# Optimization experiments

Measured on AMD Instinct MI355X. Metric: run time of the kernel, lower is better.

## Reference

```python
import jax, jax.numpy as jnp
import numpy as np

N, M, NBR = 20000, 12, 64
AF, ORIG, H, B, K = 256, 92, 256, 200, 50
N_CONV = 3
EPS = 1e-5


def _bn_train(x, gamma, beta):
    mu = x.mean(0)
    var = x.var(0)  # biased, matches torch BN normalization in train mode
    return (x - mu) * jax.lax.rsqrt(var + EPS) * gamma + beta


def _conv_layer(atom_in, nbr_fea, nbr_idx, w1, b1, w2, b2, gamma, beta):
    n, m = nbr_idx.shape
    m1 = m // 2
    atom_nbr = atom_in[nbr_idx]                     # [N, M, AF]
    atom_u = jnp.broadcast_to(atom_in[:, None, :], (n, m1, atom_in.shape[-1]))
    an1, an2 = atom_nbr[:, :m1], atom_nbr[:, m1:]
    nf1, nf2 = nbr_fea[:, :m1], nbr_fea[:, m1:]
    u1 = jnp.concatenate([atom_u, an1, nf1], axis=2)  # [N, M1, 2*AF+NBR]
    u2 = jnp.concatenate([atom_u, an2, nf2], axis=2)
    g1 = jax.nn.relu(jnp.einsum('nmf,fo->nmo', u1, w1) + b1)
    g2 = jax.nn.softplus(jnp.einsum('nmf,fo->nmo', u2, w1) + b1)
    nbr_sumed = g1.sum(1) + g2.sum(1)               # sum over all M neighbors, [N, 2*AF]
    nbr_sumed = nbr_sumed @ w2 + b2                 # [N, AF]
    nbr_sumed = _bn_train(nbr_sumed, gamma, beta)
    return jax.nn.softplus(atom_in + nbr_sumed)


def setup_inputs() -> dict:
    key = jax.random.key(0)
    ks = jax.random.split(key, 16)
    inp = {
        'atom_fea': jax.random.normal(ks[0], (N, ORIG), jnp.float32),
        'nbr_fea': jax.random.normal(ks[1], (N, M, NBR), jnp.float32),
        'nbr_fea_idx': jax.random.randint(ks[2], (N, M), 0, N),
        'M1_index': jax.random.randint(ks[3], (B * K,), 0, N),
        'seg_ids': jnp.repeat(jnp.arange(B), K),
        'm2_fea': jax.random.normal(ks[4], (B, 4), jnp.float32),
        'emb_w': jax.random.normal(ks[5], (ORIG, AF), jnp.float32) * 0.05,
        'emb_b': jnp.zeros((AF,), jnp.float32),
        'w1': jax.random.normal(ks[6], (N_CONV, 2 * AF + NBR, 2 * AF), jnp.float32) * 0.05,
        'b1': jnp.zeros((N_CONV, 2 * AF), jnp.float32),
        'w2': jax.random.normal(ks[7], (N_CONV, 2 * AF, AF), jnp.float32) * 0.05,
        'b2': jnp.zeros((N_CONV, AF), jnp.float32),
        'gamma': jnp.ones((N_CONV, AF), jnp.float32),
        'beta': jnp.zeros((N_CONV, AF), jnp.float32),
        'fc_w': jax.random.normal(ks[8], (AF + 4, H), jnp.float32) * 0.05,
        'fc_b': jnp.zeros((H,), jnp.float32),
        'out_w': jax.random.normal(ks[9], (H, 1), jnp.float32) * 0.05,
        'out_b': jnp.zeros((1,), jnp.float32),
    }
    return inp


def reference(atom_fea, nbr_fea, nbr_fea_idx, M1_index, seg_ids, m2_fea,
              emb_w, emb_b, w1, b1, w2, b2, gamma, beta,
              fc_w, fc_b, out_w, out_b):
    x = jax.nn.softplus(atom_fea @ emb_w + emb_b)           # [N, AF]
    for i in range(N_CONV):
        x = _conv_layer(x, nbr_fea, nbr_fea_idx, w1[i], b1[i], w2[i], b2[i], gamma[i], beta[i])
    m1_fea = x[M1_index]                                    # [B*K, AF]
    sums = jax.ops.segment_sum(m1_fea, seg_ids, num_segments=B)
    counts = jax.ops.segment_sum(jnp.ones((m1_fea.shape[0], 1), m1_fea.dtype), seg_ids, num_segments=B)
    crys = sums / counts                                    # per-crystal mean, [B, AF]
    crys = jnp.concatenate([crys, m2_fea], axis=1)          # [B, AF+4]
    h = jax.nn.softplus(jax.nn.softplus(crys) @ fc_w + fc_b)
    out = h @ out_w + out_b                                 # [B, 1]
    return out
```

## Files before the change

kernel.cpp:

```cpp
#include <hip/hip_runtime.h>
#include <hip/hip_bf16.h>


#define N_ATOM 20000
#define AF     256
#define F2     512
#define ORIG   92
#define ORIG_P 96
#define BB     200
#define KK     50
#define BN_EPS 1e-5f
#define ZS     132

#define OFF_B1   0
#define OFF_B2   1536
#define OFF_GAM  2304
#define OFF_BET  3072
#define OFF_EMBB 3840
#define OFF_FCB  4096
#define OFF_FCW  4352
#define OFF_OW   70912
#define OFF_OB   71168
#define OFF_M2   71169
#define N_SMALL  71969

using bf16x8 = __attribute__((ext_vector_type(8))) short;
using f32x4  = __attribute__((ext_vector_type(4))) float;

__device__ __forceinline__ float bf2f(__hip_bfloat16 v) { return __bfloat162float(v); }
__device__ __forceinline__ __hip_bfloat16 f2bf(float v) { return __float2bfloat16(v); }
__device__ __forceinline__ unsigned short f2bfbits(float f) {
    unsigned u = __float_as_uint(f);
    u += 0x7fffu + ((u >> 16) & 1u);
    return (unsigned short)(u >> 16);
}
__device__ __forceinline__ float bfbits2f(unsigned short u) {
    return __uint_as_float(((unsigned)u) << 16);
}
__device__ __forceinline__ float softplus_f(float x) {
    return fmaxf(x, 0.f) + __logf(1.f + __expf(-fabsf(x)));
}
__device__ __forceinline__ float ld_any(const void* p, long idx, bool isf32) {
    return isf32 ? ((const float*)p)[idx] : bf2f(((const __hip_bfloat16*)p)[idx]);
}

__global__ void detect_dtype(const unsigned* __restrict__ gamma_raw,
                             unsigned* __restrict__ flag) {
    unsigned u = gamma_raw[0];
    flag[0] = ((u & 0xFFFFu) == 0u) ? 1u : 0u;
}

__global__ __launch_bounds__(256) void prep_nf(const void* __restrict__ nf,
                                               const unsigned* __restrict__ dflag,
                                               unsigned* __restrict__ out) {
    bool isf32 = dflag[0] != 0u;
    int idx = blockIdx.x * 256 + threadIdx.x;
    if (idx >= N_ATOM * 12 * 64 / 4) return;
    if (isf32) {
        float4 v = ((const float4*)nf)[idx];
        out[idx * 2]     = (unsigned)f2bfbits(v.x) | ((unsigned)f2bfbits(v.y) << 16);
        out[idx * 2 + 1] = (unsigned)f2bfbits(v.z) | ((unsigned)f2bfbits(v.w) << 16);
    } else {
        uint2 v = ((const uint2*)nf)[idx];
        ((uint2*)out)[idx] = v;
    }
}

__global__ __launch_bounds__(256) void prep_pad_af(const void* __restrict__ af,
                                                   const unsigned* __restrict__ dflag,
                                                   __hip_bfloat16* __restrict__ out) {
    bool isf32 = dflag[0] != 0u;
    int i = blockIdx.x * 256 + threadIdx.x;
    if (i >= N_ATOM * ORIG_P) return;
    int r = i / ORIG_P, k = i - r * ORIG_P;
    out[i] = (k < ORIG) ? f2bf(ld_any(af, (long)r * ORIG + k, isf32)) : f2bf(0.f);
}
__global__ __launch_bounds__(256) void prep_t_emb(const void* __restrict__ w,
                                                  const unsigned* __restrict__ dflag,
                                                  __hip_bfloat16* __restrict__ out) {
    bool isf32 = dflag[0] != 0u;
    int i = blockIdx.x * 256 + threadIdx.x;
    if (i >= AF * ORIG_P) return;
    int n = i / ORIG_P, k = i - n * ORIG_P;
    out[i] = (k < ORIG) ? f2bf(ld_any(w, (long)k * AF + n, isf32)) : f2bf(0.f);
}
__global__ __launch_bounds__(256) void prep_t_w1(const void* __restrict__ w,
                                                 const unsigned* __restrict__ dflag,
                                                 __hip_bfloat16* __restrict__ out) {
    bool isf32 = dflag[0] != 0u;
    int i = blockIdx.x * 256 + threadIdx.x;
    if (i >= 3 * F2 * 576) return;
    int l = i / (F2 * 576); int rem = i - l * (F2 * 576);
    int c = rem / 576, k = rem - c * 576;
    out[i] = f2bf(ld_any(w, (long)l * 576 * F2 + (long)k * F2 + c, isf32));
}
__global__ __launch_bounds__(256) void prep_t_w2(const void* __restrict__ w,
                                                 const unsigned* __restrict__ dflag,
                                                 __hip_bfloat16* __restrict__ out) {
    bool isf32 = dflag[0] != 0u;
    int i = blockIdx.x * 256 + threadIdx.x;
    if (i >= 3 * AF * F2) return;
    int l = i / (AF * F2); int rem = i - l * (AF * F2);
    int n = rem / F2, k = rem - n * F2;
    out[i] = f2bf(ld_any(w, (long)l * F2 * AF + (long)k * AF + n, isf32));
}
__global__ __launch_bounds__(256)
void prep_smalls(const void* b1, const void* b2, const void* gam, const void* bet,
                 const void* embb, const void* fcb, const void* fcw,
                 const void* ow, const void* ob, const void* m2,
                 const unsigned* __restrict__ dflag,
                 __hip_bfloat16* __restrict__ s) {
    bool isf32 = dflag[0] != 0u;
    int i = blockIdx.x * 256 + threadIdx.x;
    if (i >= N_SMALL) return;
    float v;
    if      (i < OFF_B2)   v = ld_any(b1,   i - OFF_B1,  isf32);
    else if (i < OFF_GAM)  v = ld_any(b2,   i - OFF_B2,  isf32);
    else if (i < OFF_BET)  v = ld_any(gam,  i - OFF_GAM, isf32);
    else if (i < OFF_EMBB) v = ld_any(bet,  i - OFF_BET, isf32);
    else if (i < OFF_FCB)  v = ld_any(embb, i - OFF_EMBB,isf32);
    else if (i < OFF_OW)   v = (i < OFF_FCW) ? ld_any(fcb, i - OFF_FCB, isf32)
                                             : ld_any(fcw, i - OFF_FCW, isf32);
    else if (i < OFF_OB)   v = ld_any(ow,   i - OFF_OW,  isf32);
    else if (i < OFF_M2)   v = ld_any(ob,   i - OFF_OB,  isf32);
    else                   v = ld_any(m2,   i - OFF_M2,  isf32);
    s[i] = f2bf(v);
}

template <bool OUT_BF16>
__global__ __launch_bounds__(256)
void gemm_kernel(const __hip_bfloat16* __restrict__ A, int lda,
                 const __hip_bfloat16* __restrict__ BT, int ldb,
                 void* __restrict__ Cp, int M, int N, int K,
                 const __hip_bfloat16* __restrict__ bias, int act,
                 float* __restrict__ st) {
    __shared__ __align__(16) unsigned short sA[128 * 40];
    __shared__ __align__(16) unsigned short sB[128 * 40];
    __shared__ float sS[128], sS2[128];
    int tid  = threadIdx.x;
    int mt   = blockIdx.x, nt = blockIdx.y;
    int wave = tid >> 6, lane = tid & 63, q = lane >> 4, ln = lane & 15;
    int wr   = wave >> 1, wc = wave & 1;

    if (st && tid < 128) { sS[tid] = 0.f; sS2[tid] = 0.f; }

    f32x4 acc[4][4];
    for (int i = 0; i < 4; i++)
        for (int j = 0; j < 4; j++) acc[i][j] = (f32x4){0.f, 0.f, 0.f, 0.f};

    for (int k0 = 0; k0 < K; k0 += 32) {
        for (int i = tid; i < 512; i += 256) {
            int r = i >> 2, ch = i & 3;
            int row = mt * 128 + r;
            uint4 va = make_uint4(0u, 0u, 0u, 0u);
            if (row < M) va = *(const uint4*)(A + (size_t)row * lda + k0 + ch * 8);
            *(uint4*)(&sA[r * 40 + ch * 8]) = va;
            int n = nt * 128 + r;
            uint4 vb = *(const uint4*)(BT + (size_t)n * ldb + k0 + ch * 8);
            *(uint4*)(&sB[r * 40 + ch * 8]) = vb;
        }
        __syncthreads();
        bf16x8 af[4], bf[4];
        for (int i = 0; i < 4; i++)
            af[i] = *(const bf16x8*)(&sA[(wr * 64 + i * 16 + ln) * 40 + q * 8]);
        for (int j = 0; j < 4; j++)
            bf[j] = *(const bf16x8*)(&sB[(wc * 64 + j * 16 + ln) * 40 + q * 8]);
        for (int i = 0; i < 4; i++)
            for (int j = 0; j < 4; j++)
                acc[i][j] = __builtin_amdgcn_mfma_f32_16x16x32_bf16(af[i], bf[j], acc[i][j], 0, 0, 0);
        __syncthreads();
    }
    for (int j = 0; j < 4; j++) {
        int cl  = wc * 64 + j * 16 + ln;
        int col = nt * 128 + cl;
        float bv = bias ? bf2f(bias[col]) : 0.f;
        float ls = 0.f, ls2 = 0.f;
        for (int i = 0; i < 4; i++) {
            for (int r = 0; r < 4; r++) {
                int row = mt * 128 + wr * 64 + i * 16 + q * 4 + r;
                if (row >= M) continue;
                float v = acc[i][j][r] + bv;
                if (st) { ls += v; ls2 += v * v; }
                if (act == 1) v = softplus_f(v);
                if (OUT_BF16) ((__hip_bfloat16*)Cp)[(size_t)row * N + col] = f2bf(v);
                else          ((float*)Cp)[(size_t)row * N + col] = v;
            }
        }
        if (st) { atomicAdd(&sS[cl], ls); atomicAdd(&sS2[cl], ls2); }
    }
    if (st) {
        __syncthreads();
        if (tid < 128) {
            int col = nt * 128 + tid;
            atomicAdd(&st[col], sS[tid]);
            atomicAdd(&st[AF + col], sS2[tid]);
        }
    }
}

__global__ __launch_bounds__(256)
void conv_fused(const void* __restrict__ nf,
                const unsigned* __restrict__ dflag,
                int prepped,
                const int* __restrict__ nidx,
                const __hip_bfloat16* __restrict__ xa,
                const __hip_bfloat16* __restrict__ y,
                const __hip_bfloat16* __restrict__ w1Tl,
                __hip_bfloat16* __restrict__ ns)
{
    __shared__ __align__(16) unsigned short sNF[96 * 72];
    __shared__ __align__(16) unsigned short sR[96 * ZS];
    __shared__ int sIdx[96];
    unsigned short* sBT = sR;
    unsigned short* sZ  = sR;

    int tid = threadIdx.x;
    int ab  = blockIdx.x * 8;

    if (prepped || dflag[0] == 0u) {
        const __hip_bfloat16* nfB = (const __hip_bfloat16*)nf;
        for (int i = tid; i < 96 * 8; i += 256) {
            int r = i >> 3, ch = i & 7;
            uint4 v = *(const uint4*)(nfB + (size_t)(ab * 12 + r) * 64 + ch * 8);
            *(uint4*)(&sNF[r * 72 + ch * 8]) = v;
        }
    } else {
        const float* nfF = (const float*)nf;
        for (int i = tid; i < 96 * 8; i += 256) {
            int r = i >> 3, ch = i & 7;
            const float* src = nfF + (size_t)(ab * 12 + r) * 64 + ch * 8;
            float4 v0 = *(const float4*)(src);
            float4 v1 = *(const float4*)(src + 4);
            unsigned short* d = &sNF[r * 72 + ch * 8];
            d[0] = f2bfbits(v0.x); d[1] = f2bfbits(v0.y);
            d[2] = f2bfbits(v0.z); d[3] = f2bfbits(v0.w);
            d[4] = f2bfbits(v1.x); d[5] = f2bfbits(v1.y);
            d[6] = f2bfbits(v1.z); d[7] = f2bfbits(v1.w);
        }
    }
    if (tid < 96) sIdx[tid] = nidx[ab * 12 + tid];

    int wave = tid >> 6, lane = tid & 63, q = lane >> 4, ln = lane & 15;
    int c0 = wave * 32;
    int a  = tid >> 5, chc = tid & 31;
    int n  = ab + a;

    for (int ct = 0; ct < 4; ct++) {
        int cb = ct * 128;
        __syncthreads();
        for (int i = tid; i < 128 * 8; i += 256) {
            int c = i >> 3, ch = i & 7;
            uint4 v = *(const uint4*)(w1Tl + (size_t)(cb + c) * 576 + 512 + ch * 8);
            *(uint4*)(&sBT[c * 72 + ch * 8]) = v;
        }
        __syncthreads();

        bf16x8 bfr[2][2];
        for (int c2 = 0; c2 < 2; c2++)
            for (int ks = 0; ks < 2; ks++)
                bfr[c2][ks] = *(const bf16x8*)(&sBT[(c0 + c2 * 16 + ln) * 72 + ks * 32 + q * 8]);

        f32x4 acc[6][2];
        for (int rt = 0; rt < 6; rt++)
            for (int c2 = 0; c2 < 2; c2++) acc[rt][c2] = (f32x4){0.f, 0.f, 0.f, 0.f};
        for (int rt = 0; rt < 6; rt++) {
            bf16x8 a0 = *(const bf16x8*)(&sNF[(rt * 16 + ln) * 72 + q * 8]);
            bf16x8 a1 = *(const bf16x8*)(&sNF[(rt * 16 + ln) * 72 + 32 + q * 8]);
            acc[rt][0] = __builtin_amdgcn_mfma_f32_16x16x32_bf16(a0, bfr[0][0], acc[rt][0], 0, 0, 0);
            acc[rt][0] = __builtin_amdgcn_mfma_f32_16x16x32_bf16(a1, bfr[0][1], acc[rt][0], 0, 0, 0);
            acc[rt][1] = __builtin_amdgcn_mfma_f32_16x16x32_bf16(a0, bfr[1][0], acc[rt][1], 0, 0, 0);
            acc[rt][1] = __builtin_amdgcn_mfma_f32_16x16x32_bf16(a1, bfr[1][1], acc[rt][1], 0, 0, 0);
        }
        __syncthreads();

        for (int rt = 0; rt < 6; rt++)
            for (int c2 = 0; c2 < 2; c2++)
                for (int r = 0; r < 4; r++)
                    sZ[(rt * 16 + q * 4 + r) * ZS + c0 + c2 * 16 + ln] = f2bfbits(acc[rt][c2][r]);
        __syncthreads();

        int gc = cb + chc * 4;
        uint2 xau = *(const uint2*)(xa + (size_t)n * F2 + gc);
        float xa0 = bfbits2f((unsigned short)(xau.x & 0xffff));
        float xa1 = bfbits2f((unsigned short)(xau.x >> 16));
        float xa2 = bfbits2f((unsigned short)(xau.y & 0xffff));
        float xa3 = bfbits2f((unsigned short)(xau.y >> 16));
        float r0 = 0.f, r1 = 0.f, r2 = 0.f, r3 = 0.f;
#pragma unroll
        for (int m = 0; m < 12; m++) {
            int gi = sIdx[a * 12 + m];
            uint2 zz = *(const uint2*)(&sZ[(a * 12 + m) * ZS + chc * 4]);
            uint2 yy = *(const uint2*)(y + (size_t)gi * F2 + gc);
            float v0 = bfbits2f((unsigned short)(zz.x & 0xffff)) + xa0 +
                       bfbits2f((unsigned short)(yy.x & 0xffff));
            float v1 = bfbits2f((unsigned short)(zz.x >> 16)) + xa1 +
                       bfbits2f((unsigned short)(yy.x >> 16));
            float v2 = bfbits2f((unsigned short)(zz.y & 0xffff)) + xa2 +
                       bfbits2f((unsigned short)(yy.y & 0xffff));
            float v3 = bfbits2f((unsigned short)(zz.y >> 16)) + xa3 +
                       bfbits2f((unsigned short)(yy.y >> 16));
            if (m < 6) {
                v0 = fmaxf(v0, 0.f); v1 = fmaxf(v1, 0.f);
                v2 = fmaxf(v2, 0.f); v3 = fmaxf(v3, 0.f);
            } else {
                v0 = softplus_f(v0); v1 = softplus_f(v1);
                v2 = softplus_f(v2); v3 = softplus_f(v3);
            }
            r0 += v0; r1 += v1; r2 += v2; r3 += v3;
        }
        uint2 o;
        o.x = (unsigned)f2bfbits(r0) | ((unsigned)f2bfbits(r1) << 16);
        o.y = (unsigned)f2bfbits(r2) | ((unsigned)f2bfbits(r3) << 16);
        *(uint2*)(ns + (size_t)n * F2 + gc) = o;
    }
}

__global__ __launch_bounds__(256)
void bn_apply(const __hip_bfloat16* __restrict__ h2, const float* __restrict__ st,
              const __hip_bfloat16* __restrict__ x,
              const __hip_bfloat16* __restrict__ gamma,
              const __hip_bfloat16* __restrict__ beta,
              __hip_bfloat16* __restrict__ xo) {
    int i = (blockIdx.x * 256 + threadIdx.x) * 4;
    int c = i & 255;
    uint2 hv = *(const uint2*)(h2 + i);
    uint2 xv = *(const uint2*)(x + i);
    uint2 o;
    float r[4];
#pragma unroll
    for (int k = 0; k < 4; k++) {
        int cc = c + k;
        float mu  = st[cc] * (1.f / 20000.f);
        float var = fmaxf(st[AF + cc] * (1.f / 20000.f) - mu * mu, 0.f);
        unsigned hh = (k < 2) ? hv.x : hv.y;
        unsigned xx = (k < 2) ? xv.x : xv.y;
        float h = bfbits2f((unsigned short)((k & 1) ? (hh >> 16) : (hh & 0xffff)));
        float xf = bfbits2f((unsigned short)((k & 1) ? (xx >> 16) : (xx & 0xffff)));
        float t = (h - mu) * rsqrtf(var + BN_EPS) * bf2f(gamma[cc]) + bf2f(beta[cc]);
        r[k] = softplus_f(xf + t);
    }
    o.x = (unsigned)f2bfbits(r[0]) | ((unsigned)f2bfbits(r[1]) << 16);
    o.y = (unsigned)f2bfbits(r[2]) | ((unsigned)f2bfbits(r[3]) << 16);
    *(uint2*)(xo + i) = o;
}

__global__ __launch_bounds__(256)
void readout(const __hip_bfloat16* __restrict__ x, const int* __restrict__ m1,
             const __hip_bfloat16* __restrict__ smalls,
             const unsigned* __restrict__ dflag,
             void* __restrict__ outp) {
    __shared__ float sc[AF + 4];
    __shared__ float sred[4];
    bool isf32 = dflag[0] != 0u;
    int b = blockIdx.x, tid = threadIdx.x;
    float s = 0.f;
    for (int j = 0; j < KK; j++) {
        int row = m1[b * KK + j];
        s += bf2f(x[(size_t)row * AF + tid]);
    }
    sc[tid] = softplus_f(s * (1.f / (float)KK));
    if (tid < 4) sc[AF + tid] = softplus_f(bf2f(smalls[OFF_M2 + b * 4 + tid]));
    __syncthreads();
    float acc = bf2f(smalls[OFF_FCB + tid]);
    for (int k = 0; k < AF + 4; k++) acc += sc[k] * bf2f(smalls[OFF_FCW + k * 256 + tid]);
    float h = softplus_f(acc);
    float v = h * bf2f(smalls[OFF_OW + tid]);
    for (int off = 32; off > 0; off >>= 1) v += __shfl_down(v, off);
    if ((tid & 63) == 0) sred[tid >> 6] = v;
    __syncthreads();
    if (tid == 0) {
        float o = sred[0] + sred[1] + sred[2] + sred[3] + bf2f(smalls[OFF_OB]);
        if (isf32) ((float*)outp)[b] = o;
        else       ((__hip_bfloat16*)outp)[b] = f2bf(o);
    }
}

extern "C" void kernel_launch(void* const* d_in, const int* in_sizes, int n_in,
                              void* d_out, int out_size, void* d_ws, size_t ws_size,
                              hipStream_t stream) {
    const void* atom_fea = d_in[0];
    const void* nbr_fea  = d_in[1];
    const int*  nbr_idx  = (const int*)d_in[2];
    const int*  m1_idx   = (const int*)d_in[3];
    const void* m2_fea = d_in[5];
    const void* emb_w  = d_in[6];
    const void* emb_b  = d_in[7];
    const void* w1     = d_in[8];
    const void* b1     = d_in[9];
    const void* w2     = d_in[10];
    const void* b2     = d_in[11];
    const void* gamma  = d_in[12];
    const void* beta   = d_in[13];
    const void* fc_w   = d_in[14];
    const void* fc_b   = d_in[15];
    const void* out_w  = d_in[16];
    const void* out_b  = d_in[17];

    char* ws = (char*)d_ws;
    size_t off = 0;
    auto alloc = [&](size_t bytes) -> char* {
        char* p = ws + off;
        off += (bytes + 255) & ~(size_t)255;
        return p;
    };
    __hip_bfloat16* w1T    = (__hip_bfloat16*)alloc((size_t)3 * F2 * 576 * 2);
    __hip_bfloat16* w2T    = (__hip_bfloat16*)alloc((size_t)3 * AF * F2 * 2);
    __hip_bfloat16* smalls = (__hip_bfloat16*)alloc((size_t)N_SMALL * 2);
    __hip_bfloat16* xb0    = (__hip_bfloat16*)alloc((size_t)N_ATOM * AF * 2);
    __hip_bfloat16* xb1    = (__hip_bfloat16*)alloc((size_t)N_ATOM * AF * 2);
    char*           regX   = alloc((size_t)N_ATOM * F2 * 2);
    char*           regY   = alloc((size_t)N_ATOM * F2 * 2);
    char*           regZ   = alloc((size_t)N_ATOM * F2 * 2);
    float*          stats  = (float*)alloc((size_t)3 * 2 * AF * 4);
    unsigned*       dflag  = (unsigned*)alloc(256);
    char*           nfb    = alloc((size_t)N_ATOM * 12 * 64 * 2);
    int use_nfb = (ws_size >= off) ? 1 : 0;

    __hip_bfloat16* xa     = (__hip_bfloat16*)regX;
    __hip_bfloat16* h2     = (__hip_bfloat16*)regX;
    __hip_bfloat16* af_pad = (__hip_bfloat16*)regY;
    __hip_bfloat16* yb     = (__hip_bfloat16*)regY;
    __hip_bfloat16* embT   = (__hip_bfloat16*)regZ;
    __hip_bfloat16* nsb    = (__hip_bfloat16*)regZ;

    detect_dtype<<<1, 1, 0, stream>>>((const unsigned*)gamma, dflag);
    (void)hipMemsetAsync(stats, 0, (size_t)3 * 2 * AF * 4, stream);

    if (use_nfb)
        prep_nf<<<(N_ATOM * 12 * 64 / 4 + 255) / 256, 256, 0, stream>>>(nbr_fea, dflag,
                                                                        (unsigned*)nfb);
    prep_pad_af<<<(N_ATOM * ORIG_P + 255) / 256, 256, 0, stream>>>(atom_fea, dflag, af_pad);
    prep_t_emb<<<(AF * ORIG_P + 255) / 256, 256, 0, stream>>>(emb_w, dflag, embT);
    prep_t_w1<<<(3 * F2 * 576 + 255) / 256, 256, 0, stream>>>(w1, dflag, w1T);
    prep_t_w2<<<(3 * AF * F2 + 255) / 256, 256, 0, stream>>>(w2, dflag, w2T);
    prep_smalls<<<(N_SMALL + 255) / 256, 256, 0, stream>>>(b1, b2, gamma, beta, emb_b,
                                                           fc_b, fc_w, out_w, out_b, m2_fea,
                                                           dflag, smalls);

    dim3 g_emb((N_ATOM + 127) / 128, AF / 128);
    gemm_kernel<true><<<g_emb, 256, 0, stream>>>(af_pad, ORIG_P, embT, ORIG_P,
                                                 xb0, N_ATOM, AF, ORIG_P,
                                                 smalls + OFF_EMBB, 1, nullptr);

    const void* nf_conv = use_nfb ? (const void*)nfb : nbr_fea;

    __hip_bfloat16* xc = xb0;
    __hip_bfloat16* xn = xb1;
    for (int l = 0; l < 3; l++) {
        const __hip_bfloat16* w1Tl = w1T + (size_t)l * F2 * 576;
        dim3 gxy((N_ATOM + 127) / 128, F2 / 128);
        gemm_kernel<true><<<gxy, 256, 0, stream>>>(xc, AF, w1Tl, 576,
                                                   xa, N_ATOM, F2, AF,
                                                   smalls + OFF_B1 + l * F2, 0, nullptr);
        gemm_kernel<true><<<gxy, 256, 0, stream>>>(xc, AF, w1Tl + 256, 576,
                                                   yb, N_ATOM, F2, AF, nullptr, 0, nullptr);
        conv_fused<<<N_ATOM / 8, 256, 0, stream>>>(nf_conv, dflag, use_nfb, nbr_idx,
                                                   xa, yb, w1Tl, nsb);
        float* stl = stats + l * 2 * AF;
        dim3 gh2((N_ATOM + 127) / 128, AF / 128);
        gemm_kernel<true><<<gh2, 256, 0, stream>>>(nsb, F2, w2T + (size_t)l * AF * F2, F2,
                                                   h2, N_ATOM, AF, F2,
                                                   smalls + OFF_B2 + l * AF, 0, stl);
        bn_apply<<<(N_ATOM * AF / 4) / 256, 256, 0, stream>>>(h2, stl, xc,
                                                              smalls + OFF_GAM + l * AF,
                                                              smalls + OFF_BET + l * AF, xn);
        __hip_bfloat16* t = xc; xc = xn; xn = t;
    }
    readout<<<BB, 256, 0, stream>>>(xc, m1_idx, smalls, dflag, d_out);
}
```

Baseline: 646.4 us.

## Merge prep kernels, fuse dual node GEMMs into one, shrink conv block

Replaces the separate weight and feature prep kernels with a single prep_all launch. The two per-layer node GEMMs (self and neighbor projections) become one GEMM with N=1024 that writes an interleaved xa|y buffer. The bias add moves into conv_fused. The conv kernel now handles 4 atoms per block instead of 8 and reads the nbr_fea projection weights directly from a pre-packed global layout instead of staging them in shared memory. The separate nbr_fea bf16 conversion pass is dropped, so fp32 inputs are converted inside conv on every layer, and the smaller blocks lower shared-memory use in exchange for more blocks.

```diff
diff --git a/kernel.cpp b/kernel.cpp
--- a/kernel.cpp
+++ b/kernel.cpp
@@ -24,6 +24,14 @@
 #define OFF_M2   71169
 #define N_SMALL  71969
 
+#define S_AF   (N_ATOM * ORIG_P)
+#define S_EMB  (AF * ORIG_P)
+#define S_W12  (3 * 1024 * 256)
+#define S_W1F  (3 * 512 * 64)
+#define S_W2   (3 * AF * F2)
+#define S_SM   N_SMALL
+#define S_TOT  (S_AF + S_EMB + S_W12 + S_W1F + S_W2 + S_SM)
+
 using bf16x8 = __attribute__((ext_vector_type(8))) short;
 using f32x4  = __attribute__((ext_vector_type(4))) float;
 
@@ -50,69 +58,53 @@
     flag[0] = ((u & 0xFFFFu) == 0u) ? 1u : 0u;
 }
 
-__global__ __launch_bounds__(256) void prep_nf(const void* __restrict__ nf,
-                                               const unsigned* __restrict__ dflag,
-                                               unsigned* __restrict__ out) {
-    bool isf32 = dflag[0] != 0u;
-    int idx = blockIdx.x * 256 + threadIdx.x;
-    if (idx >= N_ATOM * 12 * 64 / 4) return;
-    if (isf32) {
-        float4 v = ((const float4*)nf)[idx];
-        out[idx * 2]     = (unsigned)f2bfbits(v.x) | ((unsigned)f2bfbits(v.y) << 16);
-        out[idx * 2 + 1] = (unsigned)f2bfbits(v.z) | ((unsigned)f2bfbits(v.w) << 16);
-    } else {
-        uint2 v = ((const uint2*)nf)[idx];
-        ((uint2*)out)[idx] = v;
-    }
-}
-
-__global__ __launch_bounds__(256) void prep_pad_af(const void* __restrict__ af,
-                                                   const unsigned* __restrict__ dflag,
-                                                   __hip_bfloat16* __restrict__ out) {
+__global__ __launch_bounds__(256)
+void prep_all(const void* af, const void* emb_w, const void* w1, const void* w2,
+              const void* b1, const void* b2, const void* gam, const void* bet,
+              const void* embb, const void* fcb, const void* fcw,
+              const void* ow, const void* ob, const void* m2,
+              const unsigned* __restrict__ dflag,
+              __hip_bfloat16* __restrict__ af_pad, __hip_bfloat16* __restrict__ embT,
+              __hip_bfloat16* __restrict__ w1T2, __hip_bfloat16* __restrict__ w1Tf,
+              __hip_bfloat16* __restrict__ w2T, __hip_bfloat16* __restrict__ smalls) {
     bool isf32 = dflag[0] != 0u;
     int i = blockIdx.x * 256 + threadIdx.x;
-    if (i >= N_ATOM * ORIG_P) return;
-    int r = i / ORIG_P, k = i - r * ORIG_P;
-    out[i] = (k < ORIG) ? f2bf(ld_any(af, (long)r * ORIG + k, isf32)) : f2bf(0.f);
-}
-__global__ __launch_bounds__(256) void prep_t_emb(const void* __restrict__ w,
-                                                  const unsigned* __restrict__ dflag,
-                                                  __hip_bfloat16* __restrict__ out) {
-    bool isf32 = dflag[0] != 0u;
-    int i = blockIdx.x * 256 + threadIdx.x;
-    if (i >= AF * ORIG_P) return;
-    int n = i / ORIG_P, k = i - n * ORIG_P;
-    out[i] = (k < ORIG) ? f2bf(ld_any(w, (long)k * AF + n, isf32)) : f2bf(0.f);
-}
-__global__ __launch_bounds__(256) void prep_t_w1(const void* __restrict__ w,
-                                                 const unsigned* __restrict__ dflag,
-                                                 __hip_bfloat16* __restrict__ out) {
-    bool isf32 = dflag[0] != 0u;
-    int i = blockIdx.x * 256 + threadIdx.x;
-    if (i >= 3 * F2 * 576) return;
-    int l = i / (F2 * 576); int rem = i - l * (F2 * 576);
-    int c = rem / 576, k = rem - c * 576;
-    out[i] = f2bf(ld_any(w, (long)l * 576 * F2 + (long)k * F2 + c, isf32));
-}
-__global__ __launch_bounds__(256) void prep_t_w2(const void* __restrict__ w,
-                                                 const unsigned* __restrict__ dflag,
-                                                 __hip_bfloat16* __restrict__ out) {
-    bool isf32 = dflag[0] != 0u;
-    int i = blockIdx.x * 256 + threadIdx.x;
-    if (i >= 3 * AF * F2) return;
-    int l = i / (AF * F2); int rem = i - l * (AF * F2);
-    int n = rem / F2, k = rem - n * F2;
-    out[i] = f2bf(ld_any(w, (long)l * F2 * AF + (long)k * AF + n, isf32));
-}
-__global__ __launch_bounds__(256)
-void prep_smalls(const void* b1, const void* b2, const void* gam, const void* bet,
-                 const void* embb, const void* fcb, const void* fcw,
-                 const void* ow, const void* ob, const void* m2,
-                 const unsigned* __restrict__ dflag,
-                 __hip_bfloat16* __restrict__ s) {
-    bool isf32 = dflag[0] != 0u;
-    int i = blockIdx.x * 256 + threadIdx.x;
-    if (i >= N_SMALL) return;
+    if (i < S_AF) {
+        int r = i / ORIG_P, k = i - r * ORIG_P;
+        af_pad[i] = (k < ORIG) ? f2bf(ld_any(af, (long)r * ORIG + k, isf32)) : f2bf(0.f);
+        return;
+    }
+    i -= S_AF;
+    if (i < S_EMB) {
+        int n = i / ORIG_P, k = i - n * ORIG_P;
+        embT[i] = (k < ORIG) ? f2bf(ld_any(emb_w, (long)k * AF + n, isf32)) : f2bf(0.f);
+        return;
+    }
+    i -= S_EMB;
+    if (i < S_W12) {
+        int l = i / (1024 * 256); int rem = i - l * (1024 * 256);
+        int c = rem / 256, k = rem - c * 256;
+        long src = (c < 512) ? ((long)(l * 576 + k) * F2 + c)
+                             : ((long)(l * 576 + 256 + k) * F2 + (c - 512));
+        w1T2[i] = f2bf(ld_any(w1, src, isf32));
+        return;
+    }
+    i -= S_W12;
+    if (i < S_W1F) {
+        int l = i / (512 * 64); int rem = i - l * (512 * 64);
+        int c = rem / 64, k = rem - c * 64;
+        w1Tf[i] = f2bf(ld_any(w1, (long)(l * 576 + 512 + k) * F2 + c, isf32));
+        return;
+    }
+    i -= S_W1F;
+    if (i < S_W2) {
+        int l = i / (AF * F2); int rem = i - l * (AF * F2);
+        int n = rem / F2, k = rem - n * F2;
+        w2T[i] = f2bf(ld_any(w2, (long)(l * F2 + k) * AF + n, isf32));
+        return;
+    }
+    i -= S_W2;
+    if (i >= S_SM) return;
     float v;
     if      (i < OFF_B2)   v = ld_any(b1,   i - OFF_B1,  isf32);
     else if (i < OFF_GAM)  v = ld_any(b2,   i - OFF_B2,  isf32);
@@ -124,14 +116,14 @@
     else if (i < OFF_OB)   v = ld_any(ow,   i - OFF_OW,  isf32);
     else if (i < OFF_M2)   v = ld_any(ob,   i - OFF_OB,  isf32);
     else                   v = ld_any(m2,   i - OFF_M2,  isf32);
-    s[i] = f2bf(v);
+    smalls[i] = f2bf(v);
 }
 
 template <bool OUT_BF16>
 __global__ __launch_bounds__(256)
 void gemm_kernel(const __hip_bfloat16* __restrict__ A, int lda,
                  const __hip_bfloat16* __restrict__ BT, int ldb,
-                 void* __restrict__ Cp, int M, int N, int K,
+                 void* __restrict__ Cp, int M, int ldc, int K,
                  const __hip_bfloat16* __restrict__ bias, int act,
                  float* __restrict__ st) {
     __shared__ __align__(16) unsigned short sA[128 * 40];
@@ -182,8 +174,8 @@
                 float v = acc[i][j][r] + bv;
                 if (st) { ls += v; ls2 += v * v; }
                 if (act == 1) v = softplus_f(v);
-                if (OUT_BF16) ((__hip_bfloat16*)Cp)[(size_t)row * N + col] = f2bf(v);
-                else          ((float*)Cp)[(size_t)row * N + col] = v;
+                if (OUT_BF16) ((__hip_bfloat16*)Cp)[(size_t)row * ldc + col] = f2bf(v);
+                else          ((float*)Cp)[(size_t)row * ldc + col] = v;
             }
         }
         if (st) { atomicAdd(&sS[cl], ls); atomicAdd(&sS2[cl], ls2); }
@@ -201,32 +193,29 @@
 __global__ __launch_bounds__(256)
 void conv_fused(const void* __restrict__ nf,
                 const unsigned* __restrict__ dflag,
-                int prepped,
                 const int* __restrict__ nidx,
-                const __hip_bfloat16* __restrict__ xa,
-                const __hip_bfloat16* __restrict__ y,
-                const __hip_bfloat16* __restrict__ w1Tl,
+                const __hip_bfloat16* __restrict__ xay,
+                const __hip_bfloat16* __restrict__ b1l,
+                const __hip_bfloat16* __restrict__ w1TfL,
                 __hip_bfloat16* __restrict__ ns)
 {
-    __shared__ __align__(16) unsigned short sNF[96 * 72];
-    __shared__ __align__(16) unsigned short sR[96 * ZS];
-    __shared__ int sIdx[96];
-    unsigned short* sBT = sR;
-    unsigned short* sZ  = sR;
+    __shared__ __align__(16) unsigned short sNF[48 * 72];
+    __shared__ __align__(16) unsigned short sZ[48 * ZS];
+    __shared__ int sIdx[48];
 
     int tid = threadIdx.x;
-    int ab  = blockIdx.x * 8;
-
-    if (prepped || dflag[0] == 0u) {
+    int ab  = blockIdx.x * 4;
+
+    if (dflag[0] == 0u) {
         const __hip_bfloat16* nfB = (const __hip_bfloat16*)nf;
-        for (int i = tid; i < 96 * 8; i += 256) {
+        for (int i = tid; i < 48 * 8; i += 256) {
             int r = i >> 3, ch = i & 7;
             uint4 v = *(const uint4*)(nfB + (size_t)(ab * 12 + r) * 64 + ch * 8);
             *(uint4*)(&sNF[r * 72 + ch * 8]) = v;
         }
     } else {
         const float* nfF = (const float*)nf;
-        for (int i = tid; i < 96 * 8; i += 256) {
+        for (int i = tid; i < 48 * 8; i += 256) {
             int r = i >> 3, ch = i & 7;
             const float* src = nfF + (size_t)(ab * 12 + r) * 64 + ch * 8;
             float4 v0 = *(const float4*)(src);
@@ -238,32 +227,26 @@
             d[6] = f2bfbits(v1.z); d[7] = f2bfbits(v1.w);
         }
     }
-    if (tid < 96) sIdx[tid] = nidx[ab * 12 + tid];
+    if (tid < 48) sIdx[tid] = nidx[ab * 12 + tid];
+    __syncthreads();
 
     int wave = tid >> 6, lane = tid & 63, q = lane >> 4, ln = lane & 15;
     int c0 = wave * 32;
-    int a  = tid >> 5, chc = tid & 31;
+    int a  = tid >> 6, cg = lane;
     int n  = ab + a;
 
     for (int ct = 0; ct < 4; ct++) {
         int cb = ct * 128;
-        __syncthreads();
-        for (int i = tid; i < 128 * 8; i += 256) {
-            int c = i >> 3, ch = i & 7;
-            uint4 v = *(const uint4*)(w1Tl + (size_t)(cb + c) * 576 + 512 + ch * 8);
-            *(uint4*)(&sBT[c * 72 + ch * 8]) = v;
-        }
-        __syncthreads();
-
         bf16x8 bfr[2][2];
         for (int c2 = 0; c2 < 2; c2++)
             for (int ks = 0; ks < 2; ks++)
-                bfr[c2][ks] = *(const bf16x8*)(&sBT[(c0 + c2 * 16 + ln) * 72 + ks * 32 + q * 8]);
-
-        f32x4 acc[6][2];
-        for (int rt = 0; rt < 6; rt++)
+                bfr[c2][ks] = *(const bf16x8*)(w1TfL +
+                    (size_t)(cb + c0 + c2 * 16 + ln) * 64 + ks * 32 + q * 8);
+
+        f32x4 acc[3][2];
+        for (int rt = 0; rt < 3; rt++)
             for (int c2 = 0; c2 < 2; c2++) acc[rt][c2] = (f32x4){0.f, 0.f, 0.f, 0.f};
-        for (int rt = 0; rt < 6; rt++) {
+        for (int rt = 0; rt < 3; rt++) {
             bf16x8 a0 = *(const bf16x8*)(&sNF[(rt * 16 + ln) * 72 + q * 8]);
             bf16x8 a1 = *(const bf16x8*)(&sNF[(rt * 16 + ln) * 72 + 32 + q * 8]);
             acc[rt][0] = __builtin_amdgcn_mfma_f32_16x16x32_bf16(a0, bfr[0][0], acc[rt][0], 0, 0, 0);
@@ -273,45 +256,35 @@
         }
         __syncthreads();
 
-        for (int rt = 0; rt < 6; rt++)
+        for (int rt = 0; rt < 3; rt++)
             for (int c2 = 0; c2 < 2; c2++)
                 for (int r = 0; r < 4; r++)
                     sZ[(rt * 16 + q * 4 + r) * ZS + c0 + c2 * 16 + ln] = f2bfbits(acc[rt][c2][r]);
         __syncthreads();
 
-        int gc = cb + chc * 4;
-        uint2 xau = *(const uint2*)(xa + (size_t)n * F2 + gc);
-        float xa0 = bfbits2f((unsigned short)(xau.x & 0xffff));
-        float xa1 = bfbits2f((unsigned short)(xau.x >> 16));
-        float xa2 = bfbits2f((unsigned short)(xau.y & 0xffff));
-        float xa3 = bfbits2f((unsigned short)(xau.y >> 16));
-        float r0 = 0.f, r1 = 0.f, r2 = 0.f, r3 = 0.f;
+        int gc = cb + cg * 2;
+        unsigned xau = *(const unsigned*)(xay + (size_t)n * 1024 + gc);
+        unsigned b1u = *(const unsigned*)(b1l + gc);
+        float xa0 = bfbits2f((unsigned short)(xau & 0xffff)) +
+                    bfbits2f((unsigned short)(b1u & 0xffff));
+        float xa1 = bfbits2f((unsigned short)(xau >> 16)) +
+                    bfbits2f((unsigned short)(b1u >> 16));
+        float r0 = 0.f, r1 = 0.f;
 #pragma unroll
         for (int m = 0; m < 12; m++) {
             int gi = sIdx[a * 12 + m];
-            uint2 zz = *(const uint2*)(&sZ[(a * 12 + m) * ZS + chc * 4]);
-            uint2 yy = *(const uint2*)(y + (size_t)gi * F2 + gc);
-            float v0 = bfbits2f((unsigned short)(zz.x & 0xffff)) + xa0 +
-                       bfbits2f((unsigned short)(yy.x & 0xffff));
-            float v1 = bfbits2f((unsigned short)(zz.x >> 16)) + xa1 +
-                       bfbits2f((unsigned short)(yy.x >> 16));
-            float v2 = bfbits2f((unsigned short)(zz.y & 0xffff)) + xa2 +
-                       bfbits2f((unsigned short)(yy.y & 0xffff));
-            float v3 = bfbits2f((unsigned short)(zz.y >> 16)) + xa3 +
-                       bfbits2f((unsigned short)(yy.y >> 16));
-            if (m < 6) {
-                v0 = fmaxf(v0, 0.f); v1 = fmaxf(v1, 0.f);
-                v2 = fmaxf(v2, 0.f); v3 = fmaxf(v3, 0.f);
-            } else {
-                v0 = softplus_f(v0); v1 = softplus_f(v1);
-                v2 = softplus_f(v2); v3 = softplus_f(v3);
-            }
-            r0 += v0; r1 += v1; r2 += v2; r3 += v3;
-        }
-        uint2 o;
-        o.x = (unsigned)f2bfbits(r0) | ((unsigned)f2bfbits(r1) << 16);
-        o.y = (unsigned)f2bfbits(r2) | ((unsigned)f2bfbits(r3) << 16);
-        *(uint2*)(ns + (size_t)n * F2 + gc) = o;
+            unsigned zz = *(const unsigned*)(&sZ[(a * 12 + m) * ZS + cg * 2]);
+            unsigned yy = *(const unsigned*)(xay + (size_t)gi * 1024 + 512 + gc);
+            float v0 = bfbits2f((unsigned short)(zz & 0xffff)) + xa0 +
+                       bfbits2f((unsigned short)(yy & 0xffff));
+            float v1 = bfbits2f((unsigned short)(zz >> 16)) + xa1 +
+                       bfbits2f((unsigned short)(yy >> 16));
+            if (m < 6) { v0 = fmaxf(v0, 0.f); v1 = fmaxf(v1, 0.f); }
+            else       { v0 = softplus_f(v0); v1 = softplus_f(v1); }
+            r0 += v0; r1 += v1;
+        }
+        unsigned o = (unsigned)f2bfbits(r0) | ((unsigned)f2bfbits(r1) << 16);
+        *(unsigned*)(ns + (size_t)n * F2 + gc) = o;
     }
 }
 
@@ -334,7 +307,7 @@
         float var = fmaxf(st[AF + cc] * (1.f / 20000.f) - mu * mu, 0.f);
         unsigned hh = (k < 2) ? hv.x : hv.y;
         unsigned xx = (k < 2) ? xv.x : xv.y;
-        float h = bfbits2f((unsigned short)((k & 1) ? (hh >> 16) : (hh & 0xffff)));
+        float h  = bfbits2f((unsigned short)((k & 1) ? (hh >> 16) : (hh & 0xffff)));
         float xf = bfbits2f((unsigned short)((k & 1) ? (xx >> 16) : (xx & 0xffff)));
         float t = (h - mu) * rsqrtf(var + BN_EPS) * bf2f(gamma[cc]) + bf2f(beta[cc]);
         r[k] = softplus_f(xf + t);
@@ -403,61 +376,46 @@
         off += (bytes + 255) & ~(size_t)255;
         return p;
     };
-    __hip_bfloat16* w1T    = (__hip_bfloat16*)alloc((size_t)3 * F2 * 576 * 2);
-    __hip_bfloat16* w2T    = (__hip_bfloat16*)alloc((size_t)3 * AF * F2 * 2);
+    __hip_bfloat16* w1T2   = (__hip_bfloat16*)alloc((size_t)S_W12 * 2);
+    __hip_bfloat16* w1Tf   = (__hip_bfloat16*)alloc((size_t)S_W1F * 2);
+    __hip_bfloat16* w2T    = (__hip_bfloat16*)alloc((size_t)S_W2 * 2);
     __hip_bfloat16* smalls = (__hip_bfloat16*)alloc((size_t)N_SMALL * 2);
     __hip_bfloat16* xb0    = (__hip_bfloat16*)alloc((size_t)N_ATOM * AF * 2);
     __hip_bfloat16* xb1    = (__hip_bfloat16*)alloc((size_t)N_ATOM * AF * 2);
-    char*           regX   = alloc((size_t)N_ATOM * F2 * 2);
-    char*           regY   = alloc((size_t)N_ATOM * F2 * 2);
+    char*           regXY  = alloc((size_t)N_ATOM * 1024 * 2);
     char*           regZ   = alloc((size_t)N_ATOM * F2 * 2);
     float*          stats  = (float*)alloc((size_t)3 * 2 * AF * 4);
     unsigned*       dflag  = (unsigned*)alloc(256);
-    char*           nfb    = alloc((size_t)N_ATOM * 12 * 64 * 2);
-    int use_nfb = (ws_size >= off) ? 1 : 0;
-
-    __hip_bfloat16* xa     = (__hip_bfloat16*)regX;
-    __hip_bfloat16* h2     = (__hip_bfloat16*)regX;
-    __hip_bfloat16* af_pad = (__hip_bfloat16*)regY;
-    __hip_bfloat16* yb     = (__hip_bfloat16*)regY;
+
+    __hip_bfloat16* xay    = (__hip_bfloat16*)regXY;
+    __hip_bfloat16* h2     = (__hip_bfloat16*)regXY;
+    __hip_bfloat16* af_pad = (__hip_bfloat16*)(regXY + (size_t)N_ATOM * F2 * 2);
     __hip_bfloat16* embT   = (__hip_bfloat16*)regZ;
     __hip_bfloat16* nsb    = (__hip_bfloat16*)regZ;
 
     detect_dtype<<<1, 1, 0, stream>>>((const unsigned*)gamma, dflag);
     (void)hipMemsetAsync(stats, 0, (size_t)3 * 2 * AF * 4, stream);
 
-    if (use_nfb)
-        prep_nf<<<(N_ATOM * 12 * 64 / 4 + 255) / 256, 256, 0, stream>>>(nbr_fea, dflag,
-                                                                        (unsigned*)nfb);
-    prep_pad_af<<<(N_ATOM * ORIG_P + 255) / 256, 256, 0, stream>>>(atom_fea, dflag, af_pad);
-    prep_t_emb<<<(AF * ORIG_P + 255) / 256, 256, 0, stream>>>(emb_w, dflag, embT);
-    prep_t_w1<<<(3 * F2 * 576 + 255) / 256, 256, 0, stream>>>(w1, dflag, w1T);
-    prep_t_w2<<<(3 * AF * F2 + 255) / 256, 256, 0, stream>>>(w2, dflag, w2T);
-    prep_smalls<<<(N_SMALL + 255) / 256, 256, 0, stream>>>(b1, b2, gamma, beta, emb_b,
-                                                           fc_b, fc_w, out_w, out_b, m2_fea,
-                                                           dflag, smalls);
-
-    dim3 g_emb((N_ATOM + 127) / 128, AF / 128);
+    prep_all<<<(S_TOT + 255) / 256, 256, 0, stream>>>(
+        atom_fea, emb_w, w1, w2, b1, b2, gamma, beta, emb_b, fc_b, fc_w,
+        out_w, out_b, m2_fea, dflag, af_pad, embT, w1T2, w1Tf, w2T, smalls);
+
+    dim3 g_emb((N_ATOM + 127) / 128, 2);
     gemm_kernel<true><<<g_emb, 256, 0, stream>>>(af_pad, ORIG_P, embT, ORIG_P,
                                                  xb0, N_ATOM, AF, ORIG_P,
                                                  smalls + OFF_EMBB, 1, nullptr);
 
-    const void* nf_conv = use_nfb ? (const void*)nfb : nbr_fea;
-
     __hip_bfloat16* xc = xb0;
     __hip_bfloat16* xn = xb1;
     for (int l = 0; l < 3; l++) {
-        const __hip_bfloat16* w1Tl = w1T + (size_t)l * F2 * 576;
-        dim3 gxy((N_ATOM + 127) / 128, F2 / 128);
-        gemm_kernel<true><<<gxy, 256, 0, stream>>>(xc, AF, w1Tl, 576,
-                                                   xa, N_ATOM, F2, AF,
-                                                   smalls + OFF_B1 + l * F2, 0, nullptr);
-        gemm_kernel<true><<<gxy, 256, 0, stream>>>(xc, AF, w1Tl + 256, 576,
-                                                   yb, N_ATOM, F2, AF, nullptr, 0, nullptr);
-        conv_fused<<<N_ATOM / 8, 256, 0, stream>>>(nf_conv, dflag, use_nfb, nbr_idx,
-                                                   xa, yb, w1Tl, nsb);
+        dim3 gxy((N_ATOM + 127) / 128, 8);
+        gemm_kernel<true><<<gxy, 256, 0, stream>>>(xc, AF, w1T2 + (size_t)l * 1024 * 256, 256,
+                                                   xay, N_ATOM, 1024, AF, nullptr, 0, nullptr);
+        conv_fused<<<N_ATOM / 4, 256, 0, stream>>>(nbr_fea, dflag, nbr_idx, xay,
+                                                   smalls + OFF_B1 + l * F2,
+                                                   w1Tf + (size_t)l * 512 * 64, nsb);
         float* stl = stats + l * 2 * AF;
-        dim3 gh2((N_ATOM + 127) / 128, AF / 128);
+        dim3 gh2((N_ATOM + 127) / 128, 2);
         gemm_kernel<true><<<gh2, 256, 0, stream>>>(nsb, F2, w2T + (size_t)l * AF * F2, F2,
                                                    h2, N_ATOM, AF, F2,
                                                    smalls + OFF_B2 + l * AF, 0, stl);
```

Measured after the change: 618.6 us. 1.05x faster.
